# Kernel tuning notes

Measured on AMD Instinct MI355X. Metric: run time of the kernel, lower is better.

Reference implementation:

```python
import jax, jax.numpy as jnp
import numpy as np

N_NODES = 50000
N_EDGES = 800000
N_GRAPHS = 64
NEG_SLOPE = 0.2
LN_EPS = 1e-5


def setup_inputs() -> dict:
    key = jax.random.key(0)
    ks = jax.random.split(key, 20)
    s = 0.1
    inp = {
        "x": jax.random.normal(ks[0], (N_NODES, 8), jnp.float32),
        "edge_index": jax.random.randint(ks[1], (2, N_EDGES), 0, N_NODES, dtype=jnp.int32),
        "edge_attr": jax.random.uniform(ks[2], (N_EDGES, 1), jnp.float32),
        "batch": jnp.sort(jax.random.randint(ks[3], (N_NODES,), 0, N_GRAPHS, dtype=jnp.int32)),
        "Wl1": jax.random.normal(ks[4], (8, 256), jnp.float32) * s,
        "Wr1": jax.random.normal(ks[5], (8, 256), jnp.float32) * s,
        "We1": jax.random.normal(ks[6], (1, 256), jnp.float32) * s,
        "att1": jax.random.normal(ks[7], (4, 64), jnp.float32) * s,
        "b1": jnp.zeros((256,), jnp.float32),
        "g1": jnp.ones((256,), jnp.float32),
        "beta1": jnp.zeros((256,), jnp.float32),
        "Wl2": jax.random.normal(ks[8], (256, 128), jnp.float32) * s,
        "Wr2": jax.random.normal(ks[9], (256, 128), jnp.float32) * s,
        "We2": jax.random.normal(ks[10], (1, 128), jnp.float32) * s,
        "att2": jax.random.normal(ks[11], (1, 128), jnp.float32) * s,
        "b2": jnp.zeros((128,), jnp.float32),
        "g2": jnp.ones((128,), jnp.float32),
        "beta2": jnp.zeros((128,), jnp.float32),
    }
    return inp


def _gatv2(x, src, dst, ea, Wl, Wr, We, att, bias, heads, ch, concat):
    """PyG GATv2Conv with add_self_loops=True (fill_value='mean' for edge_attr)."""
    n = x.shape[0]
    # self-loop edge_attr = scatter-mean of edge_attr onto target node
    deg = jax.ops.segment_sum(jnp.ones((src.shape[0],), x.dtype), dst, num_segments=n)
    loop_attr = jax.ops.segment_sum(ea, dst, num_segments=n) / jnp.maximum(deg, 1.0)[:, None]
    loop_idx = jnp.arange(n, dtype=src.dtype)
    src2 = jnp.concatenate([src, loop_idx])
    dst2 = jnp.concatenate([dst, loop_idx])
    ea2 = jnp.concatenate([ea, loop_attr], axis=0)           # (E2, edge_dim)

    xl = (x @ Wl).reshape(n, heads, ch)   # source transform
    xr = (x @ Wr).reshape(n, heads, ch)   # target transform
    e = (ea2 @ We).reshape(-1, heads, ch)

    m = xl[src2] + xr[dst2] + e           # (E2, H, C)
    m = jnp.where(m > 0, m, NEG_SLOPE * m)  # LeakyReLU(0.2)
    alpha = jnp.einsum('ehc,hc->eh', m, att)  # (E2, H)
    # softmax over edges grouped by destination node
    amax = jax.ops.segment_max(alpha, dst2, num_segments=n)
    alpha = jnp.exp(alpha - amax[dst2])
    denom = jax.ops.segment_sum(alpha, dst2, num_segments=n)
    alpha = alpha / (denom[dst2] + 1e-16)

    out = jax.ops.segment_sum(alpha[:, :, None] * xl[src2], dst2, num_segments=n)  # (N,H,C)
    out = out.reshape(n, heads * ch) if concat else out.mean(axis=1)
    return out + bias


def _layernorm(x, g, b):
    mu = x.mean(-1, keepdims=True)
    var = ((x - mu) ** 2).mean(-1, keepdims=True)
    return (x - mu) * jax.lax.rsqrt(var + LN_EPS) * g + b


def reference(x, edge_index, edge_attr, batch,
              Wl1, Wr1, We1, att1, b1, g1, beta1,
              Wl2, Wr2, We2, att2, b2, g2, beta2):
    src, dst = edge_index[0], edge_index[1]
    h = _gatv2(x, src, dst, edge_attr, Wl1, Wr1, We1, att1, b1, 4, 64, True)
    h = jax.nn.elu(_layernorm(h, g1, beta1))
    h = _gatv2(h, src, dst, edge_attr, Wl2, Wr2, We2, att2, b2, 1, 128, False)
    h = jax.nn.elu(_layernorm(h, g2, beta2))
    cnt = jax.ops.segment_sum(jnp.ones((h.shape[0],), h.dtype), batch, num_segments=N_GRAPHS)
    pooled = jax.ops.segment_sum(h, batch, num_segments=N_GRAPHS) / jnp.maximum(cnt, 1.0)[:, None]
    return pooled  # (B, 128)
```

## Files before the change

### kernel.cpp

```cpp
#include <hip/hip_runtime.h>
#include <math.h>

#define N_NODES 50000
#define N_EDGES 800000
#define N_GRAPHS 64
#define NREP 32
#define LN_EPS 1e-5f
#define SCAN_BLKS 196

typedef __attribute__((ext_vector_type(8))) short bf16x8;
typedef __attribute__((ext_vector_type(4))) float f32x4;
typedef __attribute__((ext_vector_type(2))) _Float16 half2v;

template <int CTRL>
__device__ __forceinline__ float dppadd(float v) {
  int t = __builtin_amdgcn_update_dpp(0, __float_as_int(v), CTRL, 0xF, 0xF, true);
  return v + __int_as_float(t);
}
__device__ __forceinline__ float red16d(float p) {
  p = dppadd<0xB1>(p);
  p = dppadd<0x4E>(p);
  p = dppadd<0x141>(p);
  p = dppadd<0x140>(p);
  return p;
}
__device__ __forceinline__ float red64(float p) {
  p = red16d(p);
  p += __shfl_xor(p, 16); p += __shfl_xor(p, 32);
  return p;
}

__device__ __forceinline__ unsigned f2bf(float f) {
  unsigned u = __float_as_uint(f);
  return (u + 0x7fffu + ((u >> 16) & 1u)) >> 16;
}
__device__ __forceinline__ float bflo(unsigned u) { return __uint_as_float(u << 16); }
__device__ __forceinline__ float bfhi(unsigned u) { return __uint_as_float(u & 0xffff0000u); }

__device__ __forceinline__ half2v u2h(unsigned u) {
  return __builtin_bit_cast(half2v, u);
}
__device__ __forceinline__ float dot8h(uint4 xh, unsigned w0, unsigned w1,
                                       unsigned w2, unsigned w3) {
#if __has_builtin(__builtin_amdgcn_fdot2)
  float s = __builtin_amdgcn_fdot2(u2h(xh.x), u2h(w0), 0.f, false);
  s = __builtin_amdgcn_fdot2(u2h(xh.y), u2h(w1), s, false);
  s = __builtin_amdgcn_fdot2(u2h(xh.z), u2h(w2), s, false);
  s = __builtin_amdgcn_fdot2(u2h(xh.w), u2h(w3), s, false);
  return s;
#else
  float s = 0.f;
  half2v a;
  a = u2h(xh.x); { half2v b = u2h(w0); s += (float)a.x*(float)b.x + (float)a.y*(float)b.y; }
  a = u2h(xh.y); { half2v b = u2h(w1); s += (float)a.x*(float)b.x + (float)a.y*(float)b.y; }
  a = u2h(xh.z); { half2v b = u2h(w2); s += (float)a.x*(float)b.x + (float)a.y*(float)b.y; }
  a = u2h(xh.w); { half2v b = u2h(w3); s += (float)a.x*(float)b.x + (float)a.y*(float)b.y; }
  return s;
#endif
}

__global__ void k_hist(const int* __restrict__ dst, const float* __restrict__ ea,
                       int* __restrict__ deg, float* __restrict__ easum) {
  int e = blockIdx.x * 256 + threadIdx.x;
  if (e >= N_EDGES) return;
  int d = dst[e];
  atomicAdd(&deg[d], 1);
  atomicAdd(&easum[d], ea[e]);
}

__global__ void k_scanA(const int* __restrict__ deg, int* __restrict__ part) {
  int t = threadIdx.x;
  int i = blockIdx.x * 256 + t;
  int len = (i < N_NODES) ? ((deg[i] + 4) & ~3) : 0;
  __shared__ int sm[256];
  sm[t] = len; __syncthreads();
  for (int o = 128; o > 0; o >>= 1) {
    if (t < o) sm[t] += sm[t + o];
    __syncthreads();
  }
  if (t == 0) part[blockIdx.x] = sm[0];
}
__global__ void k_scanB(const int* __restrict__ part, int* __restrict__ base) {
  int t = threadIdx.x;
  __shared__ int sm[256];
  int v = (t < SCAN_BLKS) ? part[t] : 0;
  sm[t] = v; __syncthreads();
  for (int o = 1; o < 256; o <<= 1) {
    int u = (t >= o) ? sm[t - o] : 0;
    __syncthreads();
    sm[t] += u;
    __syncthreads();
  }
  base[t] = (t == 0) ? 0 : sm[t - 1];
}
__global__ void k_scanC(const int* __restrict__ deg, const int* __restrict__ base,
                        int* __restrict__ off2) {
  int t = threadIdx.x;
  int i = blockIdx.x * 256 + t;
  int len = (i < N_NODES) ? ((deg[i] + 4) & ~3) : 0;
  __shared__ int sm[256];
  sm[t] = len; __syncthreads();
  for (int o = 1; o < 256; o <<= 1) {
    int u = (t >= o) ? sm[t - o] : 0;
    __syncthreads();
    sm[t] += u;
    __syncthreads();
  }
  int incl = sm[t];
  if (i < N_NODES) off2[i] = base[blockIdx.x] + incl - len;
  if (i == N_NODES - 1) off2[N_NODES] = base[blockIdx.x] + incl;
}

__global__ void k_self(const int* __restrict__ deg, const float* __restrict__ easum,
                       const int* __restrict__ off2,
                       int* __restrict__ ssrc, float* __restrict__ sea) {
  int n = blockIdx.x * 256 + threadIdx.x;
  if (n >= N_NODES) return;
  int b = off2[n], d = deg[n];
  ssrc[b + d] = n;
  sea[b + d]  = easum[n] / fmaxf((float)d, 1.0f);
  int pad = (d + 4) & ~3;
  for (int j = d + 1; j < pad; ++j) { ssrc[b + j] = -1; sea[b + j] = 0.f; }
}

__global__ void k_scatter(const int* __restrict__ src, const int* __restrict__ dst,
                          const float* __restrict__ ea, const int* __restrict__ off2,
                          int* __restrict__ cursor, int* __restrict__ ssrc,
                          float* __restrict__ sea) {
  int e = blockIdx.x * 256 + threadIdx.x;
  if (e >= N_EDGES) return;
  int d = dst[e];
  int pos = off2[d] + atomicAdd(&cursor[d], 1);
  ssrc[pos] = src[e];
  sea[pos]  = ea[e];
}

__global__ void k_xprep(const float* __restrict__ x, uint4* __restrict__ xh) {
  int n = blockIdx.x * 256 + threadIdx.x;
  if (n >= N_NODES) return;
  float4 a = *(const float4*)(x + n * 8);
  float4 b = *(const float4*)(x + n * 8 + 4);
  half2v p0 = {(_Float16)a.x, (_Float16)a.y};
  half2v p1 = {(_Float16)a.z, (_Float16)a.w};
  half2v p2 = {(_Float16)b.x, (_Float16)b.y};
  half2v p3 = {(_Float16)b.z, (_Float16)b.w};
  xh[n] = make_uint4(__builtin_bit_cast(unsigned, p0), __builtin_bit_cast(unsigned, p1),
                     __builtin_bit_cast(unsigned, p2), __builtin_bit_cast(unsigned, p3));
}

__global__ void k_wlprep(const float* __restrict__ Wl, unsigned* __restrict__ Wlh) {
  int kp = blockIdx.x, c = threadIdx.x;
  half2v h = {(_Float16)Wl[(2 * kp) * 256 + c], (_Float16)Wl[(2 * kp + 1) * 256 + c]};
  Wlh[kp * 256 + c] = __builtin_bit_cast(unsigned, h);
}

__global__ void k_wprep(const float* __restrict__ Wl2, const float* __restrict__ Wr2,
                        unsigned short* __restrict__ Btp) {
  int nIdx = blockIdx.x;
  int k = threadIdx.x;
  float v = (nIdx < 128) ? Wl2[k * 128 + nIdx] : Wr2[k * 128 + (nIdx - 128)];
  Btp[nIdx * 256 + k] = (unsigned short)f2bf(v);
}

__global__ __launch_bounds__(256) void k_gat1(
    const float* __restrict__ x, const uint4* __restrict__ xh16,
    const unsigned* __restrict__ Wlh,
    const float* __restrict__ Wr, const float* __restrict__ We,
    const float* __restrict__ att,
    const float* __restrict__ b1, const float* __restrict__ g1,
    const float* __restrict__ be1,
    const int* __restrict__ off2, const int* __restrict__ ssrc,
    const float* __restrict__ sea, unsigned* __restrict__ h1b) {
  int lane = threadIdx.x & 63;
  int wv = __builtin_amdgcn_readfirstlane(threadIdx.x >> 6);
  int n = blockIdx.x * 4 + wv;
  int c0 = lane * 4;

  float4 wev = *(const float4*)(We + c0);
  float4 atv = *(const float4*)(att + c0);

  float xn[8];
  {
    float4 a = *(const float4*)(x + n * 8);
    float4 b = *(const float4*)(x + n * 8 + 4);
    xn[0]=a.x; xn[1]=a.y; xn[2]=a.z; xn[3]=a.w;
    xn[4]=b.x; xn[5]=b.y; xn[6]=b.z; xn[7]=b.w;
  }
  float xr0=0.f, xr1=0.f, xr2=0.f, xr3=0.f;
#pragma unroll
  for (int k = 0; k < 8; ++k) {
    float4 wr = *(const float4*)(Wr + k * 256 + c0);
    xr0 += xn[k]*wr.x; xr1 += xn[k]*wr.y; xr2 += xn[k]*wr.z; xr3 += xn[k]*wr.w;
  }
  uint4 wk0 = *(const uint4*)(Wlh + 0 * 256 + c0);
  uint4 wk1 = *(const uint4*)(Wlh + 1 * 256 + c0);
  uint4 wk2 = *(const uint4*)(Wlh + 2 * 256 + c0);
  uint4 wk3 = *(const uint4*)(Wlh + 3 * 256 + c0);

  int beg   = __builtin_amdgcn_readfirstlane(off2[n]);
  int pairs = __builtin_amdgcn_readfirstlane((off2[n + 1] - beg) >> 1);

  float den = 0.f, ac0=0.f, ac1=0.f, ac2=0.f, ac3=0.f;

  int   sA = __builtin_amdgcn_readfirstlane(ssrc[beg]);
  int   sB = __builtin_amdgcn_readfirstlane(ssrc[beg + 1]);
  float eA = sea[beg], eB = sea[beg + 1];
  uint4 xA = xh16[max(sA, 0)];
  uint4 xB = xh16[max(sB, 0)];

  for (int p = 0; p < pairs; ++p) {
    int   csA = sA, csB = sB;
    float ceA = eA, ceB = eB;
    uint4 cxA = xA, cxB = xB;
    if (p + 1 < pairs) {
      int j = beg + 2 * (p + 1);
      sA = __builtin_amdgcn_readfirstlane(ssrc[j]);
      sB = __builtin_amdgcn_readfirstlane(ssrc[j + 1]);
      eA = sea[j];  eB = sea[j + 1];
      xA = xh16[max(sA, 0)];
      xB = xh16[max(sB, 0)];
    }
    float vA0 = dot8h(cxA, wk0.x, wk1.x, wk2.x, wk3.x);
    float vA1 = dot8h(cxA, wk0.y, wk1.y, wk2.y, wk3.y);
    float vA2 = dot8h(cxA, wk0.z, wk1.z, wk2.z, wk3.z);
    float vA3 = dot8h(cxA, wk0.w, wk1.w, wk2.w, wk3.w);
    float vB0 = dot8h(cxB, wk0.x, wk1.x, wk2.x, wk3.x);
    float vB1 = dot8h(cxB, wk0.y, wk1.y, wk2.y, wk3.y);
    float vB2 = dot8h(cxB, wk0.z, wk1.z, wk2.z, wk3.z);
    float vB3 = dot8h(cxB, wk0.w, wk1.w, wk2.w, wk3.w);

    float mA0 = vA0 + fmaf(ceA, wev.x, xr0); mA0 = fmaxf(mA0, 0.2f*mA0);
    float mA1 = vA1 + fmaf(ceA, wev.y, xr1); mA1 = fmaxf(mA1, 0.2f*mA1);
    float mA2 = vA2 + fmaf(ceA, wev.z, xr2); mA2 = fmaxf(mA2, 0.2f*mA2);
    float mA3 = vA3 + fmaf(ceA, wev.w, xr3); mA3 = fmaxf(mA3, 0.2f*mA3);
    float mB0 = vB0 + fmaf(ceB, wev.x, xr0); mB0 = fmaxf(mB0, 0.2f*mB0);
    float mB1 = vB1 + fmaf(ceB, wev.y, xr1); mB1 = fmaxf(mB1, 0.2f*mB1);
    float mB2 = vB2 + fmaf(ceB, wev.z, xr2); mB2 = fmaxf(mB2, 0.2f*mB2);
    float mB3 = vB3 + fmaf(ceB, wev.w, xr3); mB3 = fmaxf(mB3, 0.2f*mB3);

    float pA = mA0*atv.x + mA1*atv.y + mA2*atv.z + mA3*atv.w;
    float pB = mB0*atv.x + mB1*atv.y + mB2*atv.z + mB3*atv.w;
    pA = red16d(pA);
    pB = red16d(pB);

    float wA = (csA >= 0) ? __expf(pA) : 0.f;
    float wB = (csB >= 0) ? __expf(pB) : 0.f;
    den += wA + wB;
    ac0 = fmaf(wA, vA0, fmaf(wB, vB0, ac0));
    ac1 = fmaf(wA, vA1, fmaf(wB, vB1, ac1));
    ac2 = fmaf(wA, vA2, fmaf(wB, vB2, ac2));
    ac3 = fmaf(wA, vA3, fmaf(wB, vB3, ac3));
  }

  float inv = 1.0f / (den + 1e-16f);
  float4 bv = *(const float4*)(b1 + c0);
  float o0 = ac0*inv + bv.x, o1 = ac1*inv + bv.y;
  float o2 = ac2*inv + bv.z, o3 = ac3*inv + bv.w;
  float mu = red64(o0 + o1 + o2 + o3) * (1.0f / 256.0f);
  float d0 = o0-mu, d1 = o1-mu, d2 = o2-mu, d3 = o3-mu;
  float rstd = rsqrtf(red64(d0*d0 + d1*d1 + d2*d2 + d3*d3) * (1.0f/256.0f) + LN_EPS);
  float4 gv  = *(const float4*)(g1 + c0);
  float4 bev = *(const float4*)(be1 + c0);
  float y0 = d0*rstd*gv.x + bev.x; y0 = y0 > 0.f ? y0 : __expf(y0) - 1.0f;
  float y1 = d1*rstd*gv.y + bev.y; y1 = y1 > 0.f ? y1 : __expf(y1) - 1.0f;
  float y2 = d2*rstd*gv.z + bev.z; y2 = y2 > 0.f ? y2 : __expf(y2) - 1.0f;
  float y3 = d3*rstd*gv.w + bev.w; y3 = y3 > 0.f ? y3 : __expf(y3) - 1.0f;
  unsigned lo = f2bf(y0) | (f2bf(y1) << 16);
  unsigned hi = f2bf(y2) | (f2bf(y3) << 16);
  *(uint2*)(h1b + (size_t)n * 128 + lane * 2) = make_uint2(lo, hi);
}

__global__ __launch_bounds__(256) void k_gemm2(
    const unsigned* __restrict__ h1b, const unsigned short* __restrict__ Btp,
    unsigned short* __restrict__ xl2b, float* __restrict__ xr2) {
  __shared__ unsigned short Ash[64][264];
  __shared__ unsigned short Bsh[64][264];
  int t = threadIdx.x;
  int bm0 = blockIdx.x * 64;
  int n0  = blockIdx.y * 64;

#pragma unroll
  for (int i = 0; i < 8; ++i) {
    int idx = t + 256 * i;
    int row = idx >> 5, c4 = idx & 31;
    int gm = bm0 + row;
    uint4 va = (gm < N_NODES) ? *(const uint4*)(h1b + (size_t)gm * 128 + c4 * 4)
                              : make_uint4(0,0,0,0);
    *(uint4*)(&Ash[row][c4 * 8]) = va;
    uint4 vb = *(const uint4*)((const unsigned*)Btp + (size_t)(n0 + row) * 128 + c4 * 4);
    *(uint4*)(&Bsh[row][c4 * 8]) = vb;
  }
  __syncthreads();

  int lane = t & 63, w = t >> 6;
  int lm = lane & 15, lk = (lane >> 4) * 8;
  f32x4 acc[4];
#pragma unroll
  for (int i = 0; i < 4; ++i) acc[i] = (f32x4){0.f,0.f,0.f,0.f};

#pragma unroll
  for (int kk = 0; kk < 8; ++kk) {
    bf16x8 a = *(const bf16x8*)(&Ash[16*w + lm][kk*32 + lk]);
#pragma unroll
    for (int tt = 0; tt < 4; ++tt) {
      bf16x8 b = *(const bf16x8*)(&Bsh[16*tt + lm][kk*32 + lk]);
      acc[tt] = __builtin_amdgcn_mfma_f32_16x16x32_bf16(a, b, acc[tt], 0, 0, 0);
    }
  }

#pragma unroll
  for (int tt = 0; tt < 4; ++tt) {
#pragma unroll
    for (int r = 0; r < 4; ++r) {
      int node = bm0 + 16*w + (lane >> 4) * 4 + r;
      if (node < N_NODES) {
        int colg = n0 + tt * 16 + lm;
        float v = acc[tt][r];
        if (colg < 128) xl2b[(size_t)node * 128 + colg] = (unsigned short)f2bf(v);
        else            xr2 [(size_t)node * 128 + (colg - 128)] = v;
      }
    }
  }
}

__global__ __launch_bounds__(256) void k_gat2(
    const unsigned* __restrict__ xl2b, const float* __restrict__ xr2,
    const float* __restrict__ We, const float* __restrict__ att,
    const float* __restrict__ b2, const float* __restrict__ g2,
    const float* __restrict__ be2,
    const int* __restrict__ off2, const int* __restrict__ ssrc,
    const float* __restrict__ sea,
    const int* __restrict__ batch,
    float* __restrict__ pool, float* __restrict__ cnt) {
  int tid = threadIdx.x;
  int lane = tid & 63;
  int wv = __builtin_amdgcn_readfirstlane(tid >> 6);
  int row = lane >> 4, col = lane & 15;
  int n = blockIdx.x * 4 + wv;
  int c0 = col * 8;
  int cu0 = col * 4;

  float wev[8], at[8], xr[8];
  *(float4*)(wev)     = *(const float4*)(We + c0);
  *(float4*)(wev + 4) = *(const float4*)(We + c0 + 4);
  *(float4*)(at)      = *(const float4*)(att + c0);
  *(float4*)(at + 4)  = *(const float4*)(att + c0 + 4);
  *(float4*)(xr)      = *(const float4*)(xr2 + (size_t)n * 128 + c0);
  *(float4*)(xr + 4)  = *(const float4*)(xr2 + (size_t)n * 128 + c0 + 4);

  int beg   = __builtin_amdgcn_readfirstlane(off2[n]);
  int quads = __builtin_amdgcn_readfirstlane((off2[n + 1] - beg) >> 2);

  float den = 0.f;
  float ac[8] = {0,0,0,0,0,0,0,0};

  int s0 = -1, s1 = -1, s2 = -1;
  float e0 = 0.f, e1 = 0.f, e2 = 0.f;
  uint4 u0 = make_uint4(0,0,0,0), u1 = u0, u2 = u0;
  {
    s0 = ssrc[beg + row]; e0 = sea[beg + row];
    u0 = *(const uint4*)(xl2b + (size_t)max(s0, 0) * 64 + cu0);
  }
  if (quads > 1) {
    s1 = ssrc[beg + 4 + row]; e1 = sea[beg + 4 + row];
    u1 = *(const uint4*)(xl2b + (size_t)max(s1, 0) * 64 + cu0);
  }
  if (quads > 2) {
    s2 = ssrc[beg + 8 + row]; e2 = sea[beg + 8 + row];
    u2 = *(const uint4*)(xl2b + (size_t)max(s2, 0) * 64 + cu0);
  }

  for (int q = 0; q < quads; ++q) {
    int cs = s0; float ce = e0; uint4 cu = u0;
    s0 = s1; e0 = e1; u0 = u1;
    s1 = s2; e1 = e2; u1 = u2;
    if (q + 3 < quads) {
      int j = beg + (q + 3) * 4 + row;
      s2 = ssrc[j]; e2 = sea[j];
      u2 = *(const uint4*)(xl2b + (size_t)max(s2, 0) * 64 + cu0);
    }
    float v[8];
    v[0]=bflo(cu.x); v[1]=bfhi(cu.x); v[2]=bflo(cu.y); v[3]=bfhi(cu.y);
    v[4]=bflo(cu.z); v[5]=bfhi(cu.z); v[6]=bflo(cu.w); v[7]=bfhi(cu.w);
    float p = 0.f;
#pragma unroll
    for (int j = 0; j < 8; ++j) {
      float m = v[j] + fmaf(ce, wev[j], xr[j]);
      m = fmaxf(m, 0.2f * m);
      p = fmaf(m, at[j], p);
    }
    p = red16d(p);
    float w = (cs >= 0) ? __expf(p) : 0.f;
    den += w;
#pragma unroll
    for (int j = 0; j < 8; ++j) ac[j] = fmaf(w, v[j], ac[j]);
  }
  den += __shfl_xor(den, 16); den += __shfl_xor(den, 32);
#pragma unroll
  for (int j = 0; j < 8; ++j) {
    ac[j] += __shfl_xor(ac[j], 16);
    ac[j] += __shfl_xor(ac[j], 32);
  }

  float inv = 1.0f / (den + 1e-16f);
  float o[8], y[8];
  float bv[8], gv[8], bev[8];
  *(float4*)(bv)      = *(const float4*)(b2 + c0);
  *(float4*)(bv + 4)  = *(const float4*)(b2 + c0 + 4);
  *(float4*)(gv)      = *(const float4*)(g2 + c0);
  *(float4*)(gv + 4)  = *(const float4*)(g2 + c0 + 4);
  *(float4*)(bev)     = *(const float4*)(be2 + c0);
  *(float4*)(bev + 4) = *(const float4*)(be2 + c0 + 4);
  float osum = 0.f;
#pragma unroll
  for (int j = 0; j < 8; ++j) { o[j] = ac[j] * inv + bv[j]; osum += o[j]; }
  float mu = red64(osum) * (1.0f / 512.0f);
  float vsum = 0.f;
#pragma unroll
  for (int j = 0; j < 8; ++j) { o[j] -= mu; vsum += o[j] * o[j]; }
  float rstd = rsqrtf(red64(vsum) * (1.0f / 512.0f) + LN_EPS);
#pragma unroll
  for (int j = 0; j < 8; ++j) {
    float t2 = o[j] * rstd * gv[j] + bev[j];
    y[j] = t2 > 0.f ? t2 : __expf(t2) - 1.0f;
  }

  __shared__ float pbuf[4][128];
  __shared__ int gbuf[4];
  if (row == 0) {
#pragma unroll
    for (int j = 0; j < 8; ++j) pbuf[wv][c0 + j] = y[j];
  }
  if (lane == 0) gbuf[wv] = batch[n];
  __syncthreads();
  if (wv == 0) {
    int r = blockIdx.x & (NREP - 1);
    int ch = lane;
    float acc0 = pbuf[0][ch], acc1 = pbuf[0][ch+64];
    int cg = gbuf[0], cn = 1;
#pragma unroll
    for (int i = 1; i < 4; ++i) {
      if (gbuf[i] == cg) { acc0 += pbuf[i][ch]; acc1 += pbuf[i][ch+64]; cn++; }
      else {
        float* pp = pool + ((size_t)(r * N_GRAPHS + cg)) * 128;
        atomicAdd(pp + ch, acc0); atomicAdd(pp + ch + 64, acc1);
        if (lane == 0) atomicAdd(&cnt[r * N_GRAPHS + cg], (float)cn);
        cg = gbuf[i]; acc0 = pbuf[i][ch]; acc1 = pbuf[i][ch+64]; cn = 1;
      }
    }
    float* pp = pool + ((size_t)(r * N_GRAPHS + cg)) * 128;
    atomicAdd(pp + ch, acc0); atomicAdd(pp + ch + 64, acc1);
    if (lane == 0) atomicAdd(&cnt[r * N_GRAPHS + cg], (float)cn);
  }
}

__global__ void k_final(const float* __restrict__ pool, const float* __restrict__ cnt,
                        float* __restrict__ out) {
  int idx = blockIdx.x * 256 + threadIdx.x;
  if (idx >= N_GRAPHS * 128) return;
  int g = idx >> 7, c = idx & 127;
  float s = 0.f, nn = 0.f;
#pragma unroll
  for (int r = 0; r < NREP; ++r) {
    s  += pool[((size_t)(r * N_GRAPHS + g)) * 128 + c];
    nn += cnt[r * N_GRAPHS + g];
  }
  out[idx] = s / fmaxf(nn, 1.0f);
}

extern "C" void kernel_launch(void* const* d_in, const int* in_sizes, int n_in,
                              void* d_out, int out_size, void* d_ws, size_t ws_size,
                              hipStream_t stream) {
  const float* x    = (const float*)d_in[0];
  const int*   ei   = (const int*)  d_in[1];
  const float* ea   = (const float*)d_in[2];
  const int*   batch= (const int*)  d_in[3];
  const float* Wl1  = (const float*)d_in[4];
  const float* Wr1  = (const float*)d_in[5];
  const float* We1  = (const float*)d_in[6];
  const float* att1 = (const float*)d_in[7];
  const float* b1   = (const float*)d_in[8];
  const float* g1   = (const float*)d_in[9];
  const float* be1  = (const float*)d_in[10];
  const float* Wl2  = (const float*)d_in[11];
  const float* Wr2  = (const float*)d_in[12];
  const float* We2  = (const float*)d_in[13];
  const float* att2 = (const float*)d_in[14];
  const float* b2   = (const float*)d_in[15];
  const float* g2   = (const float*)d_in[16];
  const float* be2  = (const float*)d_in[17];
  const int* srcp = ei;
  const int* dstp = ei + N_EDGES;

  const int MAXE2 = N_EDGES + 4 * N_NODES;

  char* ws = (char*)d_ws;
  size_t off = 0;
  auto alloc = [&](size_t bytes) {
    char* p = ws + off; off += (bytes + 15) & ~(size_t)15; return p;
  };
  int*            deg   = (int*)           alloc((size_t)N_NODES * 4);
  float*          easum = (float*)         alloc((size_t)N_NODES * 4);
  int*            cursor= (int*)           alloc((size_t)N_NODES * 4);
  int*            off2  = (int*)           alloc((size_t)(N_NODES + 1) * 4);
  int*            part  = (int*)           alloc((size_t)256 * 4);
  int*            base  = (int*)           alloc((size_t)257 * 4);
  int*            ssrc  = (int*)           alloc((size_t)MAXE2 * 4);
  float*          sea   = (float*)         alloc((size_t)MAXE2 * 4);
  uint4*          xh16  = (uint4*)         alloc((size_t)N_NODES * 16);
  unsigned*       Wlh   = (unsigned*)      alloc((size_t)4 * 256 * 4);
  unsigned*       h1b   = (unsigned*)      alloc((size_t)N_NODES * 128 * 4);
  unsigned short* xl2b  = (unsigned short*)alloc((size_t)N_NODES * 128 * 2);
  float*          xr2   = (float*)         alloc((size_t)N_NODES * 128 * 4);
  unsigned short* Btp   = (unsigned short*)alloc((size_t)256 * 256 * 2);
  float*          pool  = (float*)         alloc((size_t)NREP * N_GRAPHS * 128 * 4);
  float*          cnt   = (float*)         alloc((size_t)NREP * N_GRAPHS * 4);

  (void)hipMemsetAsync(deg, 0, (char*)off2 - (char*)deg, stream);
  (void)hipMemsetAsync(pool, 0, ((char*)cnt + (((size_t)NREP*N_GRAPHS*4 + 15) & ~(size_t)15))
                           - (char*)pool, stream);

  k_hist   <<<N_EDGES / 256, 256, 0, stream>>>(dstp, ea, deg, easum);
  k_xprep  <<<(N_NODES + 255) / 256, 256, 0, stream>>>(x, xh16);
  k_wlprep <<<4, 256, 0, stream>>>(Wl1, Wlh);
  k_wprep  <<<256, 256, 0, stream>>>(Wl2, Wr2, Btp);
  k_scanA  <<<SCAN_BLKS, 256, 0, stream>>>(deg, part);
  k_scanB  <<<1, 256, 0, stream>>>(part, base);
  k_scanC  <<<SCAN_BLKS, 256, 0, stream>>>(deg, base, off2);
  k_self   <<<(N_NODES + 255) / 256, 256, 0, stream>>>(deg, easum, off2, ssrc, sea);
  k_scatter<<<N_EDGES / 256, 256, 0, stream>>>(srcp, dstp, ea, off2, cursor, ssrc, sea);
  k_gat1   <<<N_NODES / 4, 256, 0, stream>>>(x, xh16, Wlh, Wr1, We1, att1, b1, g1, be1,
                                             off2, ssrc, sea, h1b);
  dim3 g7((N_NODES + 63) / 64, 4);
  k_gemm2  <<<g7, 256, 0, stream>>>(h1b, Btp, xl2b, xr2);
  k_gat2   <<<N_NODES / 4, 256, 0, stream>>>((const unsigned*)xl2b, xr2, We2, att2,
                                             b2, g2, be2,
                                             off2, ssrc, sea, batch, pool, cnt);
  k_final  <<<(N_GRAPHS * 128) / 256, 256, 0, stream>>>(pool, cnt, (float*)d_out);
}
```

Before: 454.0 us.

## Schedule GAT nodes by descending degree and fuse prep and self-loop kernels

Adds a degree counting sort that builds an order array, highest-degree nodes first, so k_gat1 and k_gat2 process heavy nodes early and load imbalance at the tail shrinks. The self-loop fill moves into k_scanC, and the three weight/input prep kernels merge into one k_prep launch, cutting launch count. The cost is three extra small kernels for the sort and indirect node lookup, which loses locality between consecutive node IDs, notably for the batch-based pooling in gat2.

```diff
diff --git a/kernel.cpp b/kernel.cpp
--- a/kernel.cpp
+++ b/kernel.cpp
@@ -7,6 +7,7 @@
 #define NREP 32
 #define LN_EPS 1e-5f
 #define SCAN_BLKS 196
+#define DBINS 64
 
 typedef __attribute__((ext_vector_type(8))) short bf16x8;
 typedef __attribute__((ext_vector_type(4))) float f32x4;
@@ -68,6 +69,33 @@
   atomicAdd(&easum[d], ea[e]);
 }
 
+__global__ void k_dhist(const int* __restrict__ deg, int* __restrict__ dh) {
+  int n = blockIdx.x * 256 + threadIdx.x;
+  if (n >= N_NODES) return;
+  int bin = (DBINS - 1) - min(deg[n], DBINS - 1);
+  atomicAdd(&dh[bin], 1);
+}
+__global__ void k_dscan(const int* __restrict__ dh, int* __restrict__ dbase) {
+  int t = threadIdx.x;
+  __shared__ int sm[DBINS];
+  sm[t] = dh[t]; __syncthreads();
+  for (int o = 1; o < DBINS; o <<= 1) {
+    int u = (t >= o) ? sm[t - o] : 0;
+    __syncthreads();
+    sm[t] += u;
+    __syncthreads();
+  }
+  dbase[t] = (t == 0) ? 0 : sm[t - 1];
+}
+__global__ void k_dscatter(const int* __restrict__ deg, const int* __restrict__ dbase,
+                           int* __restrict__ dcur, int* __restrict__ order) {
+  int n = blockIdx.x * 256 + threadIdx.x;
+  if (n >= N_NODES) return;
+  int bin = (DBINS - 1) - min(deg[n], DBINS - 1);
+  int pos = dbase[bin] + atomicAdd(&dcur[bin], 1);
+  order[pos] = n;
+}
+
 __global__ void k_scanA(const int* __restrict__ deg, int* __restrict__ part) {
   int t = threadIdx.x;
   int i = blockIdx.x * 256 + t;
@@ -94,10 +122,13 @@
   base[t] = (t == 0) ? 0 : sm[t - 1];
 }
 __global__ void k_scanC(const int* __restrict__ deg, const int* __restrict__ base,
-                        int* __restrict__ off2) {
+                        const float* __restrict__ easum,
+                        int* __restrict__ off2,
+                        int* __restrict__ ssrc, float* __restrict__ sea) {
   int t = threadIdx.x;
   int i = blockIdx.x * 256 + t;
-  int len = (i < N_NODES) ? ((deg[i] + 4) & ~3) : 0;
+  int d = (i < N_NODES) ? deg[i] : 0;
+  int len = (i < N_NODES) ? ((d + 4) & ~3) : 0;
   __shared__ int sm[256];
   sm[t] = len; __syncthreads();
   for (int o = 1; o < 256; o <<= 1) {
@@ -107,20 +138,14 @@
     __syncthreads();
   }
   int incl = sm[t];
-  if (i < N_NODES) off2[i] = base[blockIdx.x] + incl - len;
+  if (i < N_NODES) {
+    int b = base[blockIdx.x] + incl - len;
+    off2[i] = b;
+    ssrc[b + d] = i;
+    sea[b + d]  = easum[i] / fmaxf((float)d, 1.0f);
+    for (int j = d + 1; j < len; ++j) { ssrc[b + j] = -1; sea[b + j] = 0.f; }
+  }
   if (i == N_NODES - 1) off2[N_NODES] = base[blockIdx.x] + incl;
-}
-
-__global__ void k_self(const int* __restrict__ deg, const float* __restrict__ easum,
-                       const int* __restrict__ off2,
-                       int* __restrict__ ssrc, float* __restrict__ sea) {
-  int n = blockIdx.x * 256 + threadIdx.x;
-  if (n >= N_NODES) return;
-  int b = off2[n], d = deg[n];
-  ssrc[b + d] = n;
-  sea[b + d]  = easum[n] / fmaxf((float)d, 1.0f);
-  int pad = (d + 4) & ~3;
-  for (int j = d + 1; j < pad; ++j) { ssrc[b + j] = -1; sea[b + j] = 0.f; }
 }
 
 __global__ void k_scatter(const int* __restrict__ src, const int* __restrict__ dst,
@@ -135,31 +160,31 @@
   sea[pos]  = ea[e];
 }
 
-__global__ void k_xprep(const float* __restrict__ x, uint4* __restrict__ xh) {
-  int n = blockIdx.x * 256 + threadIdx.x;
-  if (n >= N_NODES) return;
-  float4 a = *(const float4*)(x + n * 8);
-  float4 b = *(const float4*)(x + n * 8 + 4);
-  half2v p0 = {(_Float16)a.x, (_Float16)a.y};
-  half2v p1 = {(_Float16)a.z, (_Float16)a.w};
-  half2v p2 = {(_Float16)b.x, (_Float16)b.y};
-  half2v p3 = {(_Float16)b.z, (_Float16)b.w};
-  xh[n] = make_uint4(__builtin_bit_cast(unsigned, p0), __builtin_bit_cast(unsigned, p1),
-                     __builtin_bit_cast(unsigned, p2), __builtin_bit_cast(unsigned, p3));
-}
-
-__global__ void k_wlprep(const float* __restrict__ Wl, unsigned* __restrict__ Wlh) {
-  int kp = blockIdx.x, c = threadIdx.x;
-  half2v h = {(_Float16)Wl[(2 * kp) * 256 + c], (_Float16)Wl[(2 * kp + 1) * 256 + c]};
-  Wlh[kp * 256 + c] = __builtin_bit_cast(unsigned, h);
-}
-
-__global__ void k_wprep(const float* __restrict__ Wl2, const float* __restrict__ Wr2,
-                        unsigned short* __restrict__ Btp) {
-  int nIdx = blockIdx.x;
-  int k = threadIdx.x;
-  float v = (nIdx < 128) ? Wl2[k * 128 + nIdx] : Wr2[k * 128 + (nIdx - 128)];
-  Btp[nIdx * 256 + k] = (unsigned short)f2bf(v);
+__global__ void k_prep(const float* __restrict__ x, uint4* __restrict__ xh,
+                       const float* __restrict__ Wl1, unsigned* __restrict__ Wlh,
+                       const float* __restrict__ Wl2, const float* __restrict__ Wr2,
+                       unsigned short* __restrict__ Btp) {
+  int b = blockIdx.x, t = threadIdx.x;
+  if (b < SCAN_BLKS) {
+    int n = b * 256 + t;
+    if (n >= N_NODES) return;
+    float4 a = *(const float4*)(x + n * 8);
+    float4 c = *(const float4*)(x + n * 8 + 4);
+    half2v p0 = {(_Float16)a.x, (_Float16)a.y};
+    half2v p1 = {(_Float16)a.z, (_Float16)a.w};
+    half2v p2 = {(_Float16)c.x, (_Float16)c.y};
+    half2v p3 = {(_Float16)c.z, (_Float16)c.w};
+    xh[n] = make_uint4(__builtin_bit_cast(unsigned, p0), __builtin_bit_cast(unsigned, p1),
+                       __builtin_bit_cast(unsigned, p2), __builtin_bit_cast(unsigned, p3));
+  } else if (b < SCAN_BLKS + 4) {
+    int kp = b - SCAN_BLKS;
+    half2v h = {(_Float16)Wl1[(2 * kp) * 256 + t], (_Float16)Wl1[(2 * kp + 1) * 256 + t]};
+    Wlh[kp * 256 + t] = __builtin_bit_cast(unsigned, h);
+  } else {
+    int nIdx = b - SCAN_BLKS - 4;
+    float v = (nIdx < 128) ? Wl2[t * 128 + nIdx] : Wr2[t * 128 + (nIdx - 128)];
+    Btp[nIdx * 256 + t] = (unsigned short)f2bf(v);
+  }
 }
 
 __global__ __launch_bounds__(256) void k_gat1(
@@ -170,10 +195,11 @@
     const float* __restrict__ b1, const float* __restrict__ g1,
     const float* __restrict__ be1,
     const int* __restrict__ off2, const int* __restrict__ ssrc,
-    const float* __restrict__ sea, unsigned* __restrict__ h1b) {
+    const float* __restrict__ sea, const int* __restrict__ order,
+    unsigned* __restrict__ h1b) {
   int lane = threadIdx.x & 63;
   int wv = __builtin_amdgcn_readfirstlane(threadIdx.x >> 6);
-  int n = blockIdx.x * 4 + wv;
+  int n = __builtin_amdgcn_readfirstlane(order[blockIdx.x * 4 + wv]);
   int c0 = lane * 4;
 
   float4 wev = *(const float4*)(We + c0);
@@ -330,13 +356,13 @@
     const float* __restrict__ be2,
     const int* __restrict__ off2, const int* __restrict__ ssrc,
     const float* __restrict__ sea,
-    const int* __restrict__ batch,
+    const int* __restrict__ batch, const int* __restrict__ order,
     float* __restrict__ pool, float* __restrict__ cnt) {
   int tid = threadIdx.x;
   int lane = tid & 63;
   int wv = __builtin_amdgcn_readfirstlane(tid >> 6);
   int row = lane >> 4, col = lane & 15;
-  int n = blockIdx.x * 4 + wv;
+  int n = __builtin_amdgcn_readfirstlane(order[blockIdx.x * 4 + wv]);
   int c0 = col * 8;
   int cu0 = col * 4;
 
@@ -502,9 +528,13 @@
   int*            deg   = (int*)           alloc((size_t)N_NODES * 4);
   float*          easum = (float*)         alloc((size_t)N_NODES * 4);
   int*            cursor= (int*)           alloc((size_t)N_NODES * 4);
+  int*            dh    = (int*)           alloc((size_t)DBINS * 4);
+  int*            dcur  = (int*)           alloc((size_t)DBINS * 4);
   int*            off2  = (int*)           alloc((size_t)(N_NODES + 1) * 4);
   int*            part  = (int*)           alloc((size_t)256 * 4);
   int*            base  = (int*)           alloc((size_t)257 * 4);
+  int*            dbase = (int*)           alloc((size_t)DBINS * 4);
+  int*            order = (int*)           alloc((size_t)N_NODES * 4);
   int*            ssrc  = (int*)           alloc((size_t)MAXE2 * 4);
   float*          sea   = (float*)         alloc((size_t)MAXE2 * 4);
   uint4*          xh16  = (uint4*)         alloc((size_t)N_NODES * 16);
@@ -520,21 +550,21 @@
   (void)hipMemsetAsync(pool, 0, ((char*)cnt + (((size_t)NREP*N_GRAPHS*4 + 15) & ~(size_t)15))
                            - (char*)pool, stream);
 
-  k_hist   <<<N_EDGES / 256, 256, 0, stream>>>(dstp, ea, deg, easum);
-  k_xprep  <<<(N_NODES + 255) / 256, 256, 0, stream>>>(x, xh16);
-  k_wlprep <<<4, 256, 0, stream>>>(Wl1, Wlh);
-  k_wprep  <<<256, 256, 0, stream>>>(Wl2, Wr2, Btp);
-  k_scanA  <<<SCAN_BLKS, 256, 0, stream>>>(deg, part);
-  k_scanB  <<<1, 256, 0, stream>>>(part, base);
-  k_scanC  <<<SCAN_BLKS, 256, 0, stream>>>(deg, base, off2);
-  k_self   <<<(N_NODES + 255) / 256, 256, 0, stream>>>(deg, easum, off2, ssrc, sea);
-  k_scatter<<<N_EDGES / 256, 256, 0, stream>>>(srcp, dstp, ea, off2, cursor, ssrc, sea);
-  k_gat1   <<<N_NODES / 4, 256, 0, stream>>>(x, xh16, Wlh, Wr1, We1, att1, b1, g1, be1,
-                                             off2, ssrc, sea, h1b);
+  k_hist    <<<N_EDGES / 256, 256, 0, stream>>>(dstp, ea, deg, easum);
+  k_prep    <<<SCAN_BLKS + 4 + 256, 256, 0, stream>>>(x, xh16, Wl1, Wlh, Wl2, Wr2, Btp);
+  k_dhist   <<<SCAN_BLKS, 256, 0, stream>>>(deg, dh);
+  k_dscan   <<<1, DBINS, 0, stream>>>(dh, dbase);
+  k_dscatter<<<SCAN_BLKS, 256, 0, stream>>>(deg, dbase, dcur, order);
+  k_scanA   <<<SCAN_BLKS, 256, 0, stream>>>(deg, part);
+  k_scanB   <<<1, 256, 0, stream>>>(part, base);
+  k_scanC   <<<SCAN_BLKS, 256, 0, stream>>>(deg, base, easum, off2, ssrc, sea);
+  k_scatter <<<N_EDGES / 256, 256, 0, stream>>>(srcp, dstp, ea, off2, cursor, ssrc, sea);
+  k_gat1    <<<N_NODES / 4, 256, 0, stream>>>(x, xh16, Wlh, Wr1, We1, att1, b1, g1, be1,
+                                              off2, ssrc, sea, order, h1b);
   dim3 g7((N_NODES + 63) / 64, 4);
-  k_gemm2  <<<g7, 256, 0, stream>>>(h1b, Btp, xl2b, xr2);
-  k_gat2   <<<N_NODES / 4, 256, 0, stream>>>((const unsigned*)xl2b, xr2, We2, att2,
-                                             b2, g2, be2,
-                                             off2, ssrc, sea, batch, pool, cnt);
-  k_final  <<<(N_GRAPHS * 128) / 256, 256, 0, stream>>>(pool, cnt, (float*)d_out);
-}
+  k_gemm2   <<<g7, 256, 0, stream>>>(h1b, Btp, xl2b, xr2);
+  k_gat2    <<<N_NODES / 4, 256, 0, stream>>>((const unsigned*)xl2b, xr2, We2, att2,
+                                              b2, g2, be2,
+                                              off2, ssrc, sea, batch, order, pool, cnt);
+  k_final   <<<(N_GRAPHS * 128) / 256, 256, 0, stream>>>(pool, cnt, (float*)d_out);
+}
```

Result: slower. 661.5 us (+45.7%).
